# Performance work log

Measured on AMD Instinct MI355X. Metric: run time of the kernel, lower is better.

Reference implementation:

```python
import jax, jax.numpy as jnp
import numpy as np

DEG = 16

def setup_inputs() -> dict:
    key = jax.random.key(0)
    k1, k2 = jax.random.split(key)
    x = jax.random.uniform(k1, (2097152,), dtype=jnp.float32)  # in [0,1) subset of acos domain
    a = jax.random.normal(k2, (32, DEG), dtype=jnp.float32)
    return {"x": x, "a": a}

def reference(x, a):
    # Chebyshev basis T_k(x) = cos(k * acos(x)), shape [N, deg]
    k = jnp.arange(DEG, dtype=x.dtype)
    basis = jnp.cos(k[None, :] * jnp.arccos(x.reshape(-1))[:, None])  # [N, deg]
    coeffs = a.reshape(-1, DEG)  # [M, deg]
    # out[m, n] = sum_d coeffs[m, d] * basis[n, d]  -- a GEMM, not a 3D broadcast
    return jnp.einsum('md,nd->mn', coeffs, basis)
```

## Files before the change

### kernel.cpp

```cpp
#include <hip/hip_runtime.h>


#define DEG 16
#define M_ROWS 32
#define ELEMS_PER_THREAD 4

__global__ __launch_bounds__(256) void cheb_gemm_kernel(
    const float* __restrict__ x,
    const float* __restrict__ a,
    float* __restrict__ out,
    int n)
{
    const int i = (blockIdx.x * 256 + threadIdx.x) * ELEMS_PER_THREAD;
    if (i + ELEMS_PER_THREAD - 1 >= n) return;

    const float4 xv = *reinterpret_cast<const float4*>(x + i);
    float xs[ELEMS_PER_THREAD] = {xv.x, xv.y, xv.z, xv.w};

    float basis[ELEMS_PER_THREAD][DEG];
#pragma unroll
    for (int j = 0; j < ELEMS_PER_THREAD; ++j) {
        float t0 = 1.0f;
        float t1 = xs[j];
        basis[j][0] = t0;
        basis[j][1] = t1;
        const float two_x = xs[j] + xs[j];
#pragma unroll
        for (int k = 2; k < DEG; ++k) {
            float t2 = fmaf(two_x, t1, -t0);
            basis[j][k] = t2;
            t0 = t1;
            t1 = t2;
        }
    }

#pragma unroll 4
    for (int m = 0; m < M_ROWS; ++m) {
        float acc0 = 0.0f, acc1 = 0.0f, acc2 = 0.0f, acc3 = 0.0f;
#pragma unroll
        for (int d = 0; d < DEG; ++d) {
            const float c = a[m * DEG + d];
            acc0 = fmaf(c, basis[0][d], acc0);
            acc1 = fmaf(c, basis[1][d], acc1);
            acc2 = fmaf(c, basis[2][d], acc2);
            acc3 = fmaf(c, basis[3][d], acc3);
        }
        float4* dst = reinterpret_cast<float4*>(out + (size_t)m * (size_t)n + i);
        *dst = make_float4(acc0, acc1, acc2, acc3);
    }
}

extern "C" void kernel_launch(void* const* d_in, const int* in_sizes, int n_in,
                              void* d_out, int out_size, void* d_ws, size_t ws_size,
                              hipStream_t stream) {
    const float* x = (const float*)d_in[0];
    const float* a = (const float*)d_in[1];
    float* out = (float*)d_out;
    const int n = in_sizes[0];

    const int threads = 256;
    const int elems_per_block = threads * ELEMS_PER_THREAD;
    const int blocks = (n + elems_per_block - 1) / elems_per_block;

    cheb_gemm_kernel<<<blocks, threads, 0, stream>>>(x, a, out, n);
}
```

Before: 51.25 us.

## Split output rows across blocks, one coefficient row per block

The grid grows by a factor of 32. Each block now computes a single output row m for a 1024-element chunk of x. The Chebyshev recurrence is fused directly with that row's 16 coefficients held in registers, so the per-thread basis array and the 32-row inner loop go away. This cuts register pressure and raises the number of independent blocks, which should improve latency hiding on the write-bound output. The cost is that x is reloaded and the recurrence is recomputed 32 times, and block-launch overhead rises.

```diff
diff --git a/kernel.cpp b/kernel.cpp
--- a/kernel.cpp
+++ b/kernel.cpp
@@ -11,43 +11,38 @@
     float* __restrict__ out,
     int n)
 {
-    const int i = (blockIdx.x * 256 + threadIdx.x) * ELEMS_PER_THREAD;
+    const int b = blockIdx.x;
+    const int m = b & (M_ROWS - 1);
+    const int chunk = b >> 5;
+    const int i = chunk * (256 * ELEMS_PER_THREAD) + threadIdx.x * ELEMS_PER_THREAD;
     if (i + ELEMS_PER_THREAD - 1 >= n) return;
 
     const float4 xv = *reinterpret_cast<const float4*>(x + i);
-    float xs[ELEMS_PER_THREAD] = {xv.x, xv.y, xv.z, xv.w};
+    const float xs[ELEMS_PER_THREAD] = {xv.x, xv.y, xv.z, xv.w};
 
-    float basis[ELEMS_PER_THREAD][DEG];
+    float c[DEG];
+#pragma unroll
+    for (int d = 0; d < DEG; ++d) c[d] = a[m * DEG + d];
+
+    float acc[ELEMS_PER_THREAD];
 #pragma unroll
     for (int j = 0; j < ELEMS_PER_THREAD; ++j) {
         float t0 = 1.0f;
         float t1 = xs[j];
-        basis[j][0] = t0;
-        basis[j][1] = t1;
         const float two_x = xs[j] + xs[j];
+        float s = fmaf(c[1], t1, c[0]);
 #pragma unroll
         for (int k = 2; k < DEG; ++k) {
-            float t2 = fmaf(two_x, t1, -t0);
-            basis[j][k] = t2;
+            const float t2 = fmaf(two_x, t1, -t0);
+            s = fmaf(c[k], t2, s);
             t0 = t1;
             t1 = t2;
         }
+        acc[j] = s;
     }
 
-#pragma unroll 4
-    for (int m = 0; m < M_ROWS; ++m) {
-        float acc0 = 0.0f, acc1 = 0.0f, acc2 = 0.0f, acc3 = 0.0f;
-#pragma unroll
-        for (int d = 0; d < DEG; ++d) {
-            const float c = a[m * DEG + d];
-            acc0 = fmaf(c, basis[0][d], acc0);
-            acc1 = fmaf(c, basis[1][d], acc1);
-            acc2 = fmaf(c, basis[2][d], acc2);
-            acc3 = fmaf(c, basis[3][d], acc3);
-        }
-        float4* dst = reinterpret_cast<float4*>(out + (size_t)m * (size_t)n + i);
-        *dst = make_float4(acc0, acc1, acc2, acc3);
-    }
+    float4* dst = reinterpret_cast<float4*>(out + (size_t)m * (size_t)n + i);
+    *dst = make_float4(acc[0], acc[1], acc[2], acc[3]);
 }
 
 extern "C" void kernel_launch(void* const* d_in, const int* in_sizes, int n_in,
@@ -60,7 +55,8 @@
 
     const int threads = 256;
     const int elems_per_block = threads * ELEMS_PER_THREAD;
-    const int blocks = (n + elems_per_block - 1) / elems_per_block;
+    const int chunks = (n + elems_per_block - 1) / elems_per_block;
+    const int blocks = chunks * M_ROWS;
 
     cheb_gemm_kernel<<<blocks, threads, 0, stream>>>(x, a, out, n);
 }
```

Measured after the change: 66.69 us. 30.1% more time.

## Use packed FP32 FMA with two elements per thread and higher occupancy

Applied to the files above, without the earlier changes.

Basis values are stored as float pairs, and the 16-term dot product uses inline v_pk_fma_f32 with coefficient pairs held in scalar registers. The result is two partial sums per output that are added at the end. Elements per thread drop from 4 to 2, which doubles the block count, and launch bounds now request 8 waves per SIMD. The output stores become float2 instead of float4. The 256 MB output write probably bounds the kernel, so the packed math may matter little, while the narrower stores could hurt write efficiency.

```diff
diff --git a/kernel.cpp b/kernel.cpp
--- a/kernel.cpp
+++ b/kernel.cpp
@@ -3,32 +3,35 @@
 
 #define DEG 16
 #define M_ROWS 32
-#define ELEMS_PER_THREAD 4
+#define EPT 2
 
-__global__ __launch_bounds__(256) void cheb_gemm_kernel(
+typedef __attribute__((ext_vector_type(2))) float f32x2;
+
+__global__ __launch_bounds__(256, 8) void cheb_gemm_kernel(
     const float* __restrict__ x,
     const float* __restrict__ a,
     float* __restrict__ out,
     int n)
 {
-    const int i = (blockIdx.x * 256 + threadIdx.x) * ELEMS_PER_THREAD;
-    if (i + ELEMS_PER_THREAD - 1 >= n) return;
+    const int i = (blockIdx.x * 256 + threadIdx.x) * EPT;
+    if (i + EPT - 1 >= n) return;
 
-    const float4 xv = *reinterpret_cast<const float4*>(x + i);
-    float xs[ELEMS_PER_THREAD] = {xv.x, xv.y, xv.z, xv.w};
+    const float2 xv = *reinterpret_cast<const float2*>(x + i);
+    const float xs[EPT] = {xv.x, xv.y};
 
-    float basis[ELEMS_PER_THREAD][DEG];
+    f32x2 bp[EPT][DEG / 2];
 #pragma unroll
-    for (int j = 0; j < ELEMS_PER_THREAD; ++j) {
+    for (int j = 0; j < EPT; ++j) {
         float t0 = 1.0f;
         float t1 = xs[j];
-        basis[j][0] = t0;
-        basis[j][1] = t1;
         const float two_x = xs[j] + xs[j];
+        bp[j][0].x = t0;
+        bp[j][0].y = t1;
 #pragma unroll
         for (int k = 2; k < DEG; ++k) {
-            float t2 = fmaf(two_x, t1, -t0);
-            basis[j][k] = t2;
+            const float t2 = fmaf(two_x, t1, -t0);
+            if (k & 1) bp[j][k >> 1].y = t2;
+            else       bp[j][k >> 1].x = t2;
             t0 = t1;
             t1 = t2;
         }
@@ -36,17 +39,21 @@
 
 #pragma unroll 4
     for (int m = 0; m < M_ROWS; ++m) {
-        float acc0 = 0.0f, acc1 = 0.0f, acc2 = 0.0f, acc3 = 0.0f;
+        const float* am = a + m * DEG;
+        f32x2 acc0, acc1;
+        {
+            const f32x2 cp = *reinterpret_cast<const f32x2*>(am);
+            asm("v_pk_mul_f32 %0, %1, %2" : "=v"(acc0) : "s"(cp), "v"(bp[0][0]));
+            asm("v_pk_mul_f32 %0, %1, %2" : "=v"(acc1) : "s"(cp), "v"(bp[1][0]));
+        }
 #pragma unroll
-        for (int d = 0; d < DEG; ++d) {
-            const float c = a[m * DEG + d];
-            acc0 = fmaf(c, basis[0][d], acc0);
-            acc1 = fmaf(c, basis[1][d], acc1);
-            acc2 = fmaf(c, basis[2][d], acc2);
-            acc3 = fmaf(c, basis[3][d], acc3);
+        for (int dd = 1; dd < DEG / 2; ++dd) {
+            const f32x2 cp = *reinterpret_cast<const f32x2*>(am + 2 * dd);
+            asm("v_pk_fma_f32 %0, %1, %2, %0" : "+v"(acc0) : "s"(cp), "v"(bp[0][dd]));
+            asm("v_pk_fma_f32 %0, %1, %2, %0" : "+v"(acc1) : "s"(cp), "v"(bp[1][dd]));
         }
-        float4* dst = reinterpret_cast<float4*>(out + (size_t)m * (size_t)n + i);
-        *dst = make_float4(acc0, acc1, acc2, acc3);
+        float2* dst = reinterpret_cast<float2*>(out + (size_t)m * (size_t)n + i);
+        *dst = make_float2(acc0.x + acc0.y, acc1.x + acc1.y);
     }
 }
 
@@ -59,7 +66,7 @@
     const int n = in_sizes[0];
 
     const int threads = 256;
-    const int elems_per_block = threads * ELEMS_PER_THREAD;
+    const int elems_per_block = threads * EPT;
     const int blocks = (n + elems_per_block - 1) / elems_per_block;
 
     cheb_gemm_kernel<<<blocks, threads, 0, stream>>>(x, a, out, n);
```

After: 56.95 us. 11.1% more time.
